# Kernel tuning notes

Measured on AMD Instinct MI355X. Metric: run time of the kernel, lower is better.

The kernel has to match this reference:

```python
import jax, jax.numpy as jnp
import numpy as np

D = 1024
H = 16
DH = D // H  # 64
FF_H = 4096
EPS = 1e-5


def layernorm(x, gamma, beta):
    mu = jnp.mean(x, axis=-1, keepdims=True)
    var = jnp.var(x, axis=-1, keepdims=True)
    return (x - mu) * jax.lax.rsqrt(var + EPS) * gamma + beta


def setup_inputs() -> dict:
    key = jax.random.key(0)
    ks = jax.random.split(key, 12)
    B, S = 2, 2048
    q = jax.random.normal(ks[0], (B, S, D), dtype=jnp.float32)
    k = jax.random.normal(ks[1], (B, S, D), dtype=jnp.float32)
    v = jax.random.normal(ks[2], (B, S, D), dtype=jnp.float32)
    time_lengths = jax.random.randint(ks[3], (B,), 0, S)
    mask = jnp.zeros((1, 1, S, S), dtype=jnp.float32)
    sc = 0.02
    Wq = jax.random.normal(ks[4], (D, D), dtype=jnp.float32) * sc
    Wk = jax.random.normal(ks[5], (D, D), dtype=jnp.float32) * sc
    Wv = jax.random.normal(ks[6], (D, D), dtype=jnp.float32) * sc
    Wd = jax.random.normal(ks[7], (D, D), dtype=jnp.float32) * sc
    W1 = jax.random.normal(ks[8], (D, FF_H), dtype=jnp.float32) * sc
    b1 = jnp.zeros((FF_H,), dtype=jnp.float32)
    W2 = jax.random.normal(ks[9], (FF_H, D), dtype=jnp.float32) * sc
    b2 = jnp.zeros((D,), dtype=jnp.float32)
    g1 = jnp.ones((D,), dtype=jnp.float32)
    be1 = jnp.zeros((D,), dtype=jnp.float32)
    g2 = jnp.ones((D,), dtype=jnp.float32)
    be2 = jnp.zeros((D,), dtype=jnp.float32)
    return {"q": q, "k": k, "v": v, "time_lengths": time_lengths, "mask": mask,
            "Wq": Wq, "Wk": Wk, "Wv": Wv, "Wd": Wd,
            "W1": W1, "b1": b1, "W2": W2, "b2": b2,
            "g1": g1, "be1": be1, "g2": g2, "be2": be2}


def reference(q, k, v, time_lengths, mask, Wq, Wk, Wv, Wd, W1, b1, W2, b2, g1, be1, g2, be2):
    B, S, _ = q.shape
    scale = jnp.sqrt(jnp.float32(DH))
    # project and split heads: [B,H,S,DH]
    qh = (q @ Wq).reshape(B, S, H, DH).transpose(0, 2, 1, 3)
    kh = (k @ Wk).reshape(B, S, H, DH).transpose(0, 2, 1, 3)
    vh = (v @ Wv).reshape(B, S, H, DH).transpose(0, 2, 1, 3)
    score = jnp.einsum('bhqd,bhkd->bhqk', qh, kh) / scale + mask
    attn = jax.nn.softmax(score, axis=-1)
    z = jnp.einsum('bhqk,bhkd->bhqd', attn, vh)
    z = z.transpose(0, 2, 1, 3).reshape(B, S, D)
    z = z @ Wd
    # Add & LayerNorm 1 (note: original applies LN to attn out, then adds q)
    x = layernorm(z, g1, be1) + q
    # FF (dropout is identity in eval)
    ff = jax.nn.relu(x @ W1 + b1) @ W2 + b2
    return layernorm(ff + x, g2, be2)
```

## Files before the change

kernel.cpp:

```cpp
#include <hip/hip_runtime.h>
#include <hip/hip_bf16.h>


#define SEQ 2048
#define DM  1024
#define LNEPS 1e-5f

typedef __attribute__((ext_vector_type(8))) short bf16x8;
typedef __attribute__((ext_vector_type(4))) float f32x4;

#define GAS __attribute__((address_space(1)))
#define LAS __attribute__((address_space(3)))

static __device__ __forceinline__ void gl_lds16(const unsigned short* g, unsigned short* l) {
    __builtin_amdgcn_global_load_lds((const GAS void*)g, (LAS void*)l, 16, 0, 0);
}

static __device__ __forceinline__ unsigned short f2bf(float f) {
    unsigned u = __builtin_bit_cast(unsigned, f);
    u += 0x7fffu + ((u >> 16) & 1u);
    return (unsigned short)(u >> 16);
}

__global__ __launch_bounds__(256) void gemm_bf16(
    const unsigned short* __restrict__ A, const unsigned short* __restrict__ Bt,
    float* __restrict__ Cf, unsigned short* __restrict__ Cb,
    int M, int N, int Klen, int lda, int ldb,
    size_t sA, size_t sB, size_t sC,
    const float* __restrict__ bias, int ep)
{
    __shared__ unsigned short As[128 * 32];
    __shared__ unsigned short Bs[128 * 32];

    const int t = threadIdx.x, lane = t & 63, w = t >> 6;
    const int wm = w >> 1, wn = w & 1;
    const int m0 = blockIdx.y * 128, n0 = blockIdx.x * 128;
    A  += (size_t)blockIdx.z * sA;
    Bt += (size_t)blockIdx.z * sB;
    const size_t cbase = (size_t)blockIdx.z * sC;
    const int l15 = lane & 15, l16 = lane >> 4;
    const int ar = lane >> 2, ac = (lane & 3) * 8;

    f32x4 acc[4][4];
    #pragma unroll
    for (int i = 0; i < 4; i++)
        #pragma unroll
        for (int j = 0; j < 4; j++)
            acc[i][j] = (f32x4){0.f, 0.f, 0.f, 0.f};

    for (int k0 = 0; k0 < Klen; k0 += 32) {
        __syncthreads();
        #pragma unroll
        for (int i = 0; i < 2; i++) {
            const int rg = w * 2 + i;
            gl_lds16(&A [(size_t)(m0 + rg * 16 + ar) * lda + k0 + ac], &As[rg * 512]);
            gl_lds16(&Bt[(size_t)(n0 + rg * 16 + ar) * ldb + k0 + ac], &Bs[rg * 512]);
        }
        __syncthreads();

        bf16x8 af[4], bfr[4];
        #pragma unroll
        for (int i = 0; i < 4; i++) {
            af[i]  = *(const bf16x8*)&As[(wm * 64 + i * 16 + l15) * 32 + l16 * 8];
            bfr[i] = *(const bf16x8*)&Bs[(wn * 64 + i * 16 + l15) * 32 + l16 * 8];
        }
        #pragma unroll
        for (int mi = 0; mi < 4; mi++)
            #pragma unroll
            for (int ni = 0; ni < 4; ni++)
                acc[mi][ni] = __builtin_amdgcn_mfma_f32_16x16x32_bf16(
                    af[mi], bfr[ni], acc[mi][ni], 0, 0, 0);
    }

    #pragma unroll
    for (int ni = 0; ni < 4; ni++) {
        const int col = n0 + wn * 64 + ni * 16 + l15;
        const float bv = (ep && blockIdx.z == 0) ? bias[col] : 0.f;
        #pragma unroll
        for (int mi = 0; mi < 4; mi++) {
            #pragma unroll
            for (int r = 0; r < 4; r++) {
                const int row = m0 + wm * 64 + mi * 16 + l16 * 4 + r;
                float vv = acc[mi][ni][r] + bv;
                if (ep == 2) vv = fmaxf(vv, 0.f);
                if (Cf) Cf[cbase + (size_t)row * N + col] = vv;
                else    Cb[cbase + (size_t)row * N + col] = f2bf(vv);
            }
        }
    }
}

__global__ __launch_bounds__(256) void attn_mfma(
    const unsigned short* __restrict__ qh, const unsigned short* __restrict__ kh,
    const unsigned short* __restrict__ vhT, const float* __restrict__ mask,
    unsigned short* __restrict__ z)
{
    __shared__ unsigned short Qs[64 * 64];
    __shared__ unsigned short Ks[64 * 64];
    __shared__ unsigned short Vst[64 * 64];
    __shared__ unsigned short Ps[64 * 72];

    const int t = threadIdx.x, lane = t & 63, w = t >> 6;
    const int bid = blockIdx.x;
    const int qt = bid >> 5, h = bid & 15, b = (bid >> 4) & 1;
    const int q0 = qt * 64, qr = w * 16;
    const int l15 = lane & 15, l16 = lane >> 4;

    const int lr = lane >> 3;
    const int gc = ((lane & 7) ^ lr) * 8;

    const size_t qbase = (size_t)(b * SEQ + q0) * DM + h * 64;
    const size_t kbase = (size_t)(b * SEQ) * DM + h * 64;
    const size_t vbase = (size_t)((b * 16 + h) * 64) * SEQ;

    #pragma unroll
    for (int i = 0; i < 2; i++) {
        const int rg = w * 2 + i;
        gl_lds16(&qh[qbase + (size_t)(rg * 8 + lr) * DM + gc], &Qs[rg * 512]);
    }
    __syncthreads();

    const int sw0 = ((l16    ) ^ (l15 & 7)) * 8;
    const int sw1 = ((l16 + 4) ^ (l15 & 7)) * 8;
    const bf16x8 bQ0 = *(const bf16x8*)&Qs[(qr + l15) * 64 + sw0];
    const bf16x8 bQ1 = *(const bf16x8*)&Qs[(qr + l15) * 64 + sw1];

    const float* mrow = mask + (size_t)(q0 + qr + l15) * SEQ;

    float m_i = -1e30f, l_i = 0.f;
    f32x4 o4[4];
    #pragma unroll
    for (int mi = 0; mi < 4; mi++) o4[mi] = (f32x4){0.f, 0.f, 0.f, 0.f};

    for (int kt = 0; kt < SEQ / 64; kt++) {
        const int k0 = kt * 64;
        __syncthreads();
        #pragma unroll
        for (int i = 0; i < 2; i++) {
            const int rg = w * 2 + i;
            gl_lds16(&kh [kbase + (size_t)(k0 + rg * 8 + lr) * DM + gc], &Ks[rg * 512]);
            gl_lds16(&vhT[vbase + (size_t)(rg * 8 + lr) * SEQ + k0 + gc], &Vst[rg * 512]);
        }
        __syncthreads();

        f32x4 s4[4];
        #pragma unroll
        for (int ki = 0; ki < 4; ki++) {
            const int r = ki * 16 + l15;
            const bf16x8 aK0 = *(const bf16x8*)&Ks[r * 64 + sw0];
            const bf16x8 aK1 = *(const bf16x8*)&Ks[r * 64 + sw1];
            f32x4 a0 = (f32x4){0.f, 0.f, 0.f, 0.f};
            a0 = __builtin_amdgcn_mfma_f32_16x16x32_bf16(aK0, bQ0, a0, 0, 0, 0);
            s4[ki] = __builtin_amdgcn_mfma_f32_16x16x32_bf16(aK1, bQ1, a0, 0, 0, 0);
        }

        float sv[4][4];
        #pragma unroll
        for (int ki = 0; ki < 4; ki++) {
            const float4 mv = *(const float4*)&mrow[k0 + ki * 16 + l16 * 4];
            sv[ki][0] = s4[ki][0] * 0.125f + mv.x;
            sv[ki][1] = s4[ki][1] * 0.125f + mv.y;
            sv[ki][2] = s4[ki][2] * 0.125f + mv.z;
            sv[ki][3] = s4[ki][3] * 0.125f + mv.w;
        }

        float rm = -1e30f;
        #pragma unroll
        for (int ki = 0; ki < 4; ki++)
            #pragma unroll
            for (int r = 0; r < 4; r++) rm = fmaxf(rm, sv[ki][r]);
        rm = fmaxf(rm, __shfl_xor(rm, 16));
        rm = fmaxf(rm, __shfl_xor(rm, 32));
        const float mnew  = fmaxf(m_i, rm);
        const float alpha = __expf(m_i - mnew);
        m_i = mnew;

        float ps = 0.f;
        #pragma unroll
        for (int ki = 0; ki < 4; ki++) {
            float p[4];
            #pragma unroll
            for (int r = 0; r < 4; r++) { p[r] = __expf(sv[ki][r] - mnew); ps += p[r]; }
            ushort4 pk;
            pk.x = f2bf(p[0]); pk.y = f2bf(p[1]); pk.z = f2bf(p[2]); pk.w = f2bf(p[3]);
            *(ushort4*)&Ps[(qr + l15) * 72 + ki * 16 + l16 * 4] = pk;
        }
        ps += __shfl_xor(ps, 16);
        ps += __shfl_xor(ps, 32);
        l_i = l_i * alpha + ps;
        #pragma unroll
        for (int mi = 0; mi < 4; mi++)
            #pragma unroll
            for (int r = 0; r < 4; r++) o4[mi][r] *= alpha;

        const bf16x8 bP0 = *(const bf16x8*)&Ps[(qr + l15) * 72 + l16 * 8];
        const bf16x8 bP1 = *(const bf16x8*)&Ps[(qr + l15) * 72 + 32 + l16 * 8];
        #pragma unroll
        for (int mi = 0; mi < 4; mi++) {
            const int r = mi * 16 + l15;
            const bf16x8 aV0 = *(const bf16x8*)&Vst[r * 64 + sw0];
            const bf16x8 aV1 = *(const bf16x8*)&Vst[r * 64 + sw1];
            o4[mi] = __builtin_amdgcn_mfma_f32_16x16x32_bf16(aV0, bP0, o4[mi], 0, 0, 0);
            o4[mi] = __builtin_amdgcn_mfma_f32_16x16x32_bf16(aV1, bP1, o4[mi], 0, 0, 0);
        }
    }

    const float inv = 1.f / l_i;
    #pragma unroll
    for (int mi = 0; mi < 4; mi++) {
        ushort4 ok;
        ok.x = f2bf(o4[mi][0] * inv); ok.y = f2bf(o4[mi][1] * inv);
        ok.z = f2bf(o4[mi][2] * inv); ok.w = f2bf(o4[mi][3] * inv);
        *(ushort4*)&z[(size_t)(b * SEQ + q0 + qr + l15) * DM + h * 64 + mi * 16 + l16 * 4] = ok;
    }
}

__global__ __launch_bounds__(256) void cast3_bf16(
    const float* __restrict__ a0, const float* __restrict__ a1, const float* __restrict__ a2,
    unsigned short* __restrict__ out)
{
    const float* src = blockIdx.z == 0 ? a0 : (blockIdx.z == 1 ? a1 : a2);
    const size_t i = ((size_t)blockIdx.x * 256 + threadIdx.x) * 4;
    const float4 v = *(const float4*)&src[i];
    ushort4 o; o.x = f2bf(v.x); o.y = f2bf(v.y); o.z = f2bf(v.z); o.w = f2bf(v.w);
    *(ushort4*)&out[(size_t)blockIdx.z * ((size_t)SEQ * 2 * DM) + i] = o;
}

__global__ __launch_bounds__(256) void transpose_cast(
    const float* __restrict__ W, unsigned short* __restrict__ Wt, int K, int N)
{
    __shared__ float ts[64][65];
    const int n0 = blockIdx.x * 64, k0 = blockIdx.y * 64;
    const int t = threadIdx.x, r = t >> 4, c4 = (t & 15) * 4;
    #pragma unroll
    for (int i = 0; i < 4; i++) {
        const float4 v = *(const float4*)&W[(size_t)(k0 + r + i * 16) * N + n0 + c4];
        ts[r + i * 16][c4 + 0] = v.x; ts[r + i * 16][c4 + 1] = v.y;
        ts[r + i * 16][c4 + 2] = v.z; ts[r + i * 16][c4 + 3] = v.w;
    }
    __syncthreads();
    #pragma unroll
    for (int i = 0; i < 4; i++) {
        const int n = r + i * 16;
        ushort4 o;
        o.x = f2bf(ts[c4 + 0][n]); o.y = f2bf(ts[c4 + 1][n]);
        o.z = f2bf(ts[c4 + 2][n]); o.w = f2bf(ts[c4 + 3][n]);
        *(ushort4*)&Wt[(size_t)(n0 + n) * K + k0 + c4] = o;
    }
}

__global__ __launch_bounds__(256) void transpose_v(
    const unsigned short* __restrict__ vh, unsigned short* __restrict__ vhT)
{
    __shared__ unsigned short ts[64][80];
    const int s0 = blockIdx.x * 64, h = blockIdx.y, b = blockIdx.z;
    const int t = threadIdx.x, rr = t >> 3, c8 = (t & 7) * 8;
    #pragma unroll
    for (int i = 0; i < 2; i++) {
        const int srow = rr + i * 32;
        *(uint4*)&ts[srow][c8] = *(const uint4*)&vh[(size_t)(b * SEQ + s0 + srow) * DM + h * 64 + c8];
    }
    __syncthreads();
    #pragma unroll
    for (int i = 0; i < 2; i++) {
        const int dr = rr + i * 32;
        ushort4 ov0, ov1;
        ov0.x = ts[c8 + 0][dr]; ov0.y = ts[c8 + 1][dr];
        ov0.z = ts[c8 + 2][dr]; ov0.w = ts[c8 + 3][dr];
        ov1.x = ts[c8 + 4][dr]; ov1.y = ts[c8 + 5][dr];
        ov1.z = ts[c8 + 6][dr]; ov1.w = ts[c8 + 7][dr];
        *(ushort4*)&vhT[(size_t)((b * 16 + h) * 64 + dr) * SEQ + s0 + c8] = ov0;
        *(ushort4*)&vhT[(size_t)((b * 16 + h) * 64 + dr) * SEQ + s0 + c8 + 4] = ov1;
    }
}

__global__ __launch_bounds__(256) void ln_res(
    const float* __restrict__ a, const float* __restrict__ a2,
    const float* __restrict__ r,
    const float* __restrict__ g, const float* __restrict__ be,
    float* __restrict__ out, unsigned short* __restrict__ outb, int mode)
{
    __shared__ float redls[8];
    const int row = blockIdx.x, t = threadIdx.x;
    const size_t base = (size_t)row * DM;

    float vals[4], s = 0.f, sq = 0.f;
    #pragma unroll
    for (int i = 0; i < 4; i++) {
        const int c = t + 256 * i;
        float x = a[base + c];
        if (a2) x += a2[base + c];
        if (mode == 1) x += r[base + c];
        vals[i] = x; s += x; sq += x * x;
    }
    #pragma unroll
    for (int off = 32; off > 0; off >>= 1) { s += __shfl_down(s, off); sq += __shfl_down(sq, off); }
    if ((t & 63) == 0) { redls[t >> 6] = s; redls[4 + (t >> 6)] = sq; }
    __syncthreads();
    s  = redls[0] + redls[1] + redls[2] + redls[3];
    sq = redls[4] + redls[5] + redls[6] + redls[7];

    const float mu  = s * (1.f / 1024.f);
    const float var = sq * (1.f / 1024.f) - mu * mu;
    const float rs  = rsqrtf(var + LNEPS);
    #pragma unroll
    for (int i = 0; i < 4; i++) {
        const int c = t + 256 * i;
        float y = (vals[i] - mu) * rs * g[c] + be[c];
        if (mode == 0) y += r[base + c];
        out[base + c] = y;
        if (outb) outb[base + c] = f2bf(y);
    }
}

extern "C" void kernel_launch(void* const* d_in, const int* in_sizes, int n_in,
                              void* d_out, int out_size, void* d_ws, size_t ws_size,
                              hipStream_t stream)
{
    const float* q    = (const float*)d_in[0];
    const float* k    = (const float*)d_in[1];
    const float* v    = (const float*)d_in[2];
    const float* mask = (const float*)d_in[4];
    const float* Wq   = (const float*)d_in[5];
    const float* Wk   = (const float*)d_in[6];
    const float* Wv   = (const float*)d_in[7];
    const float* Wd   = (const float*)d_in[8];
    const float* W1   = (const float*)d_in[9];
    const float* b1   = (const float*)d_in[10];
    const float* W2   = (const float*)d_in[11];
    const float* b2   = (const float*)d_in[12];
    const float* g1   = (const float*)d_in[13];
    const float* be1  = (const float*)d_in[14];
    const float* g2   = (const float*)d_in[15];
    const float* be2  = (const float*)d_in[16];
    float* out = (float*)d_out;

    char* WS = (char*)d_ws;
    const size_t MiB = 1u << 20;
    const size_t ND  = (size_t)4096 * 1024;

    unsigned short* qb  = (unsigned short*)(WS + 0);
    unsigned short* vhT = (unsigned short*)(WS + 0);
    unsigned short* zb  = (unsigned short*)(WS + 8 * MiB);
    unsigned short* xb  = (unsigned short*)(WS + 16 * MiB);
    unsigned short* Wqt = (unsigned short*)(WS + 24 * MiB);
    unsigned short* Wdt = (unsigned short*)(WS + 30 * MiB);
    unsigned short* W1t = (unsigned short*)(WS + 32 * MiB);
    unsigned short* W2t = (unsigned short*)(WS + 40 * MiB);
    unsigned short* qh  = (unsigned short*)(WS + 48 * MiB);
    float*          zd0 = (float*)(WS + 48 * MiB);
    float*          zd1 = (float*)(WS + 64 * MiB);
    float*          x   = (float*)(WS + 80 * MiB);
    unsigned short* h1  = (unsigned short*)(WS + 96 * MiB);
    float*          y0  = (float*)(WS + 48 * MiB);
    float*          y1  = (float*)(WS + 64 * MiB);

    unsigned short* kh = qh + ND;
    unsigned short* vh = qh + 2 * ND;

    const dim3 blk(256);

    cast3_bf16<<<dim3(4096, 1, 3), blk, 0, stream>>>(q, k, v, qb);
    transpose_cast<<<dim3(16, 16), blk, 0, stream>>>(Wq, Wqt,                   1024, 1024);
    transpose_cast<<<dim3(16, 16), blk, 0, stream>>>(Wk, Wqt + 1024 * 1024,     1024, 1024);
    transpose_cast<<<dim3(16, 16), blk, 0, stream>>>(Wv, Wqt + 2 * 1024 * 1024, 1024, 1024);
    transpose_cast<<<dim3(16, 16), blk, 0, stream>>>(Wd, Wdt, 1024, 1024);
    transpose_cast<<<dim3(64, 16), blk, 0, stream>>>(W1, W1t, 1024, 4096);
    transpose_cast<<<dim3(16, 64), blk, 0, stream>>>(W2, W2t, 4096, 1024);

    gemm_bf16<<<dim3(8, 32, 3), blk, 0, stream>>>(qb, Wqt, nullptr, qh,
        4096, 1024, 1024, 1024, 1024, ND, (size_t)1024 * 1024, ND, nullptr, 0);

    transpose_v<<<dim3(32, 16, 2), blk, 0, stream>>>(vh, vhT);

    attn_mfma<<<dim3(1024), blk, 0, stream>>>(qh, kh, vhT, mask, zb);

    gemm_bf16<<<dim3(8, 32, 2), blk, 0, stream>>>(zb, Wdt, zd0, nullptr,
        4096, 1024, 512, 1024, 1024, 512, 512, ND, nullptr, 0);

    ln_res<<<dim3(4096), blk, 0, stream>>>(zd0, zd1, q, g1, be1, x, xb, 0);

    gemm_bf16<<<dim3(32, 32, 1), blk, 0, stream>>>(xb, W1t, nullptr, h1,
        4096, 4096, 1024, 1024, 1024, 0, 0, 0, b1, 2);
    gemm_bf16<<<dim3(8, 32, 2), blk, 0, stream>>>(h1, W2t, y0, nullptr,
        4096, 1024, 2048, 4096, 4096, 2048, 2048, ND, b2, 1);

    ln_res<<<dim3(4096), blk, 0, stream>>>(y0, y1, x, g2, be2, out, nullptr, 1);
}
```

Baseline: 502.0 us.

## Double-buffer K/V tiles in attention and switch softmax to exp2 domain

The attention kernel now double-buffers the K and V LDS tiles, prefetching the next tile while computing on the current one, with one barrier per iteration instead of two. Softmax runs in base 2: the score scale folds in log2(e) and a new pre-pass multiplies the mask by log2(e) into workspace. P is packed to bf16 by truncation using a byte permute instead of round-to-nearest. The four square weight transposes are merged into one launch. The cost is an extra mask-scaling pass over a 16 MiB buffer, larger LDS use, and slightly less accurate P values.

```diff
diff --git a/kernel.cpp b/kernel.cpp
--- a/kernel.cpp
+++ b/kernel.cpp
@@ -5,6 +5,7 @@
 #define SEQ 2048
 #define DM  1024
 #define LNEPS 1e-5f
+#define SCL  0.1803368801f
 
 typedef __attribute__((ext_vector_type(8))) short bf16x8;
 typedef __attribute__((ext_vector_type(4))) float f32x4;
@@ -20,6 +21,11 @@
     unsigned u = __builtin_bit_cast(unsigned, f);
     u += 0x7fffu + ((u >> 16) & 1u);
     return (unsigned short)(u >> 16);
+}
+
+static __device__ __forceinline__ unsigned pack_bf16_trunc(float a, float b) {
+    return __builtin_amdgcn_perm(__builtin_bit_cast(unsigned, b),
+                                 __builtin_bit_cast(unsigned, a), 0x07060302u);
 }
 
 __global__ __launch_bounds__(256) void gemm_bf16(
@@ -92,12 +98,12 @@
 
 __global__ __launch_bounds__(256) void attn_mfma(
     const unsigned short* __restrict__ qh, const unsigned short* __restrict__ kh,
-    const unsigned short* __restrict__ vhT, const float* __restrict__ mask,
+    const unsigned short* __restrict__ vhT, const float* __restrict__ maskl,
     unsigned short* __restrict__ z)
 {
     __shared__ unsigned short Qs[64 * 64];
-    __shared__ unsigned short Ks[64 * 64];
-    __shared__ unsigned short Vst[64 * 64];
+    __shared__ unsigned short Ks[2][64 * 64];
+    __shared__ unsigned short Vst[2][64 * 64];
     __shared__ unsigned short Ps[64 * 72];
 
     const int t = threadIdx.x, lane = t & 63, w = t >> 6;
@@ -116,7 +122,9 @@
     #pragma unroll
     for (int i = 0; i < 2; i++) {
         const int rg = w * 2 + i;
-        gl_lds16(&qh[qbase + (size_t)(rg * 8 + lr) * DM + gc], &Qs[rg * 512]);
+        gl_lds16(&qh [qbase + (size_t)(rg * 8 + lr) * DM + gc], &Qs[rg * 512]);
+        gl_lds16(&kh [kbase + (size_t)(rg * 8 + lr) * DM + gc], &Ks[0][rg * 512]);
+        gl_lds16(&vhT[vbase + (size_t)(rg * 8 + lr) * SEQ + gc], &Vst[0][rg * 512]);
     }
     __syncthreads();
 
@@ -125,7 +133,7 @@
     const bf16x8 bQ0 = *(const bf16x8*)&Qs[(qr + l15) * 64 + sw0];
     const bf16x8 bQ1 = *(const bf16x8*)&Qs[(qr + l15) * 64 + sw1];
 
-    const float* mrow = mask + (size_t)(q0 + qr + l15) * SEQ;
+    const float* mrow = maskl + (size_t)(q0 + qr + l15) * SEQ;
 
     float m_i = -1e30f, l_i = 0.f;
     f32x4 o4[4];
@@ -134,21 +142,29 @@
 
     for (int kt = 0; kt < SEQ / 64; kt++) {
         const int k0 = kt * 64;
-        __syncthreads();
-        #pragma unroll
-        for (int i = 0; i < 2; i++) {
-            const int rg = w * 2 + i;
-            gl_lds16(&kh [kbase + (size_t)(k0 + rg * 8 + lr) * DM + gc], &Ks[rg * 512]);
-            gl_lds16(&vhT[vbase + (size_t)(rg * 8 + lr) * SEQ + k0 + gc], &Vst[rg * 512]);
-        }
-        __syncthreads();
+        const int cur = kt & 1;
+
+        float4 mv[4];
+        #pragma unroll
+        for (int ki = 0; ki < 4; ki++)
+            mv[ki] = *(const float4*)&mrow[k0 + ki * 16 + l16 * 4];
+
+        if (kt < SEQ / 64 - 1) {
+            const int k1 = k0 + 64, nb = cur ^ 1;
+            #pragma unroll
+            for (int i = 0; i < 2; i++) {
+                const int rg = w * 2 + i;
+                gl_lds16(&kh [kbase + (size_t)(k1 + rg * 8 + lr) * DM + gc], &Ks[nb][rg * 512]);
+                gl_lds16(&vhT[vbase + (size_t)(rg * 8 + lr) * SEQ + k1 + gc], &Vst[nb][rg * 512]);
+            }
+        }
 
         f32x4 s4[4];
         #pragma unroll
         for (int ki = 0; ki < 4; ki++) {
             const int r = ki * 16 + l15;
-            const bf16x8 aK0 = *(const bf16x8*)&Ks[r * 64 + sw0];
-            const bf16x8 aK1 = *(const bf16x8*)&Ks[r * 64 + sw1];
+            const bf16x8 aK0 = *(const bf16x8*)&Ks[cur][r * 64 + sw0];
+            const bf16x8 aK1 = *(const bf16x8*)&Ks[cur][r * 64 + sw1];
             f32x4 a0 = (f32x4){0.f, 0.f, 0.f, 0.f};
             a0 = __builtin_amdgcn_mfma_f32_16x16x32_bf16(aK0, bQ0, a0, 0, 0, 0);
             s4[ki] = __builtin_amdgcn_mfma_f32_16x16x32_bf16(aK1, bQ1, a0, 0, 0, 0);
@@ -157,11 +173,10 @@
         float sv[4][4];
         #pragma unroll
         for (int ki = 0; ki < 4; ki++) {
-            const float4 mv = *(const float4*)&mrow[k0 + ki * 16 + l16 * 4];
-            sv[ki][0] = s4[ki][0] * 0.125f + mv.x;
-            sv[ki][1] = s4[ki][1] * 0.125f + mv.y;
-            sv[ki][2] = s4[ki][2] * 0.125f + mv.z;
-            sv[ki][3] = s4[ki][3] * 0.125f + mv.w;
+            sv[ki][0] = s4[ki][0] * SCL + mv[ki].x;
+            sv[ki][1] = s4[ki][1] * SCL + mv[ki].y;
+            sv[ki][2] = s4[ki][2] * SCL + mv[ki].z;
+            sv[ki][3] = s4[ki][3] * SCL + mv[ki].w;
         }
 
         float rm = -1e30f;
@@ -172,7 +187,7 @@
         rm = fmaxf(rm, __shfl_xor(rm, 16));
         rm = fmaxf(rm, __shfl_xor(rm, 32));
         const float mnew  = fmaxf(m_i, rm);
-        const float alpha = __expf(m_i - mnew);
+        const float alpha = exp2f(m_i - mnew);
         m_i = mnew;
 
         float ps = 0.f;
@@ -180,10 +195,11 @@
         for (int ki = 0; ki < 4; ki++) {
             float p[4];
             #pragma unroll
-            for (int r = 0; r < 4; r++) { p[r] = __expf(sv[ki][r] - mnew); ps += p[r]; }
-            ushort4 pk;
-            pk.x = f2bf(p[0]); pk.y = f2bf(p[1]); pk.z = f2bf(p[2]); pk.w = f2bf(p[3]);
-            *(ushort4*)&Ps[(qr + l15) * 72 + ki * 16 + l16 * 4] = pk;
+            for (int r = 0; r < 4; r++) { p[r] = exp2f(sv[ki][r] - mnew); ps += p[r]; }
+            uint2 pk;
+            pk.x = pack_bf16_trunc(p[0], p[1]);
+            pk.y = pack_bf16_trunc(p[2], p[3]);
+            *(uint2*)&Ps[(qr + l15) * 72 + ki * 16 + l16 * 4] = pk;
         }
         ps += __shfl_xor(ps, 16);
         ps += __shfl_xor(ps, 32);
@@ -198,11 +214,13 @@
         #pragma unroll
         for (int mi = 0; mi < 4; mi++) {
             const int r = mi * 16 + l15;
-            const bf16x8 aV0 = *(const bf16x8*)&Vst[r * 64 + sw0];
-            const bf16x8 aV1 = *(const bf16x8*)&Vst[r * 64 + sw1];
+            const bf16x8 aV0 = *(const bf16x8*)&Vst[cur][r * 64 + sw0];
+            const bf16x8 aV1 = *(const bf16x8*)&Vst[cur][r * 64 + sw1];
             o4[mi] = __builtin_amdgcn_mfma_f32_16x16x32_bf16(aV0, bP0, o4[mi], 0, 0, 0);
             o4[mi] = __builtin_amdgcn_mfma_f32_16x16x32_bf16(aV1, bP1, o4[mi], 0, 0, 0);
         }
+
+        __syncthreads();
     }
 
     const float inv = 1.f / l_i;
@@ -224,6 +242,43 @@
     const float4 v = *(const float4*)&src[i];
     ushort4 o; o.x = f2bf(v.x); o.y = f2bf(v.y); o.z = f2bf(v.z); o.w = f2bf(v.w);
     *(ushort4*)&out[(size_t)blockIdx.z * ((size_t)SEQ * 2 * DM) + i] = o;
+}
+
+__global__ __launch_bounds__(256) void scale_mask(
+    const float* __restrict__ m, float* __restrict__ o)
+{
+    const size_t i = ((size_t)blockIdx.x * 256 + threadIdx.x) * 4;
+    float4 v = *(const float4*)&m[i];
+    v.x *= 1.44269504f; v.y *= 1.44269504f; v.z *= 1.44269504f; v.w *= 1.44269504f;
+    *(float4*)&o[i] = v;
+}
+
+__global__ __launch_bounds__(256) void transpose_cast4(
+    const float* __restrict__ p0, const float* __restrict__ p1,
+    const float* __restrict__ p2, const float* __restrict__ p3,
+    unsigned short* __restrict__ Wt)
+{
+    const float* W = blockIdx.z == 0 ? p0 : (blockIdx.z == 1 ? p1 :
+                     (blockIdx.z == 2 ? p2 : p3));
+    unsigned short* dst = Wt + (size_t)blockIdx.z * 1024 * 1024;
+    __shared__ float ts[64][65];
+    const int n0 = blockIdx.x * 64, k0 = blockIdx.y * 64;
+    const int t = threadIdx.x, r = t >> 4, c4 = (t & 15) * 4;
+    #pragma unroll
+    for (int i = 0; i < 4; i++) {
+        const float4 v = *(const float4*)&W[(size_t)(k0 + r + i * 16) * 1024 + n0 + c4];
+        ts[r + i * 16][c4 + 0] = v.x; ts[r + i * 16][c4 + 1] = v.y;
+        ts[r + i * 16][c4 + 2] = v.z; ts[r + i * 16][c4 + 3] = v.w;
+    }
+    __syncthreads();
+    #pragma unroll
+    for (int i = 0; i < 4; i++) {
+        const int n = r + i * 16;
+        ushort4 o;
+        o.x = f2bf(ts[c4 + 0][n]); o.y = f2bf(ts[c4 + 1][n]);
+        o.z = f2bf(ts[c4 + 2][n]); o.w = f2bf(ts[c4 + 3][n]);
+        *(ushort4*)&dst[(size_t)(n0 + n) * 1024 + k0 + c4] = o;
+    }
 }
 
 __global__ __launch_bounds__(256) void transpose_cast(
@@ -344,7 +399,6 @@
     unsigned short* zb  = (unsigned short*)(WS + 8 * MiB);
     unsigned short* xb  = (unsigned short*)(WS + 16 * MiB);
     unsigned short* Wqt = (unsigned short*)(WS + 24 * MiB);
-    unsigned short* Wdt = (unsigned short*)(WS + 30 * MiB);
     unsigned short* W1t = (unsigned short*)(WS + 32 * MiB);
     unsigned short* W2t = (unsigned short*)(WS + 40 * MiB);
     unsigned short* qh  = (unsigned short*)(WS + 48 * MiB);
@@ -352,19 +406,19 @@
     float*          zd1 = (float*)(WS + 64 * MiB);
     float*          x   = (float*)(WS + 80 * MiB);
     unsigned short* h1  = (unsigned short*)(WS + 96 * MiB);
+    float*          mkl = (float*)(WS + 96 * MiB);
     float*          y0  = (float*)(WS + 48 * MiB);
     float*          y1  = (float*)(WS + 64 * MiB);
 
-    unsigned short* kh = qh + ND;
-    unsigned short* vh = qh + 2 * ND;
+    unsigned short* kh  = qh + ND;
+    unsigned short* vh  = qh + 2 * ND;
+    unsigned short* Wdt = Wqt + 3 * 1024 * 1024;
 
     const dim3 blk(256);
 
     cast3_bf16<<<dim3(4096, 1, 3), blk, 0, stream>>>(q, k, v, qb);
-    transpose_cast<<<dim3(16, 16), blk, 0, stream>>>(Wq, Wqt,                   1024, 1024);
-    transpose_cast<<<dim3(16, 16), blk, 0, stream>>>(Wk, Wqt + 1024 * 1024,     1024, 1024);
-    transpose_cast<<<dim3(16, 16), blk, 0, stream>>>(Wv, Wqt + 2 * 1024 * 1024, 1024, 1024);
-    transpose_cast<<<dim3(16, 16), blk, 0, stream>>>(Wd, Wdt, 1024, 1024);
+    scale_mask<<<dim3(4096), blk, 0, stream>>>(mask, mkl);
+    transpose_cast4<<<dim3(16, 16, 4), blk, 0, stream>>>(Wq, Wk, Wv, Wd, Wqt);
     transpose_cast<<<dim3(64, 16), blk, 0, stream>>>(W1, W1t, 1024, 4096);
     transpose_cast<<<dim3(16, 64), blk, 0, stream>>>(W2, W2t, 4096, 1024);
 
@@ -373,7 +427,7 @@
 
     transpose_v<<<dim3(32, 16, 2), blk, 0, stream>>>(vh, vhT);
 
-    attn_mfma<<<dim3(1024), blk, 0, stream>>>(qh, kh, vhT, mask, zb);
+    attn_mfma<<<dim3(1024), blk, 0, stream>>>(qh, kh, vhT, mkl, zb);
 
     gemm_bf16<<<dim3(8, 32, 2), blk, 0, stream>>>(zb, Wdt, zd0, nullptr,
         4096, 1024, 512, 1024, 1024, 512, 512, ND, nullptr, 0);
```

Measured after the change: 538.3 us. 1.07x slower.
